# Optimization experiments

Measured on AMD Instinct MI355X. Metric: run time of the kernel, lower is better.

The kernel has to match this reference:

```python
import math
import jax, jax.numpy as jnp
import numpy as np

B, S, M, D, H, FF = 2, 2048, 64, 1024, 16, 4096
HD = D // H


def setup_inputs() -> dict:
    key = jax.random.key(0)
    ks = jax.random.split(key, 16)
    w = lambda k, shape: jax.random.normal(k, shape, dtype=jnp.float32) * 0.02
    # RoPE angles: theta_i = pos / 10000^(2i/head_dim)
    inv_freq = 1.0 / (10000.0 ** (jnp.arange(0, HD, 2, dtype=jnp.float32) / HD))
    ang = jnp.arange(S, dtype=jnp.float32)[:, None] * inv_freq[None, :]  # (S, HD//2)
    return {
        "tgt": jax.random.normal(ks[0], (B, S, D), dtype=jnp.float32),
        "memory": jax.random.normal(ks[1], (B, M, D), dtype=jnp.float32),
        "rope_cos": jnp.cos(ang),
        "rope_sin": jnp.sin(ang),
        "W_qkv": w(ks[2], (D, 3 * D)), "b_qkv": jnp.zeros((3 * D,), jnp.float32),
        "W_o": w(ks[3], (D, D)), "b_o": jnp.zeros((D,), jnp.float32),
        "Wq_c": w(ks[4], (D, D)), "bq_c": jnp.zeros((D,), jnp.float32),
        "Wk_c": w(ks[5], (D, D)), "bk_c": jnp.zeros((D,), jnp.float32),
        "Wv_c": w(ks[6], (D, D)), "bv_c": jnp.zeros((D,), jnp.float32),
        "W_co": w(ks[7], (D, D)), "b_co": jnp.zeros((D,), jnp.float32),
        "W1": w(ks[8], (D, FF)), "b1": jnp.zeros((FF,), jnp.float32),
        "W2": w(ks[9], (FF, D)), "b2": jnp.zeros((D,), jnp.float32),
        "g1": jnp.ones((D,), jnp.float32), "be1": jnp.zeros((D,), jnp.float32),
        "g2": jnp.ones((D,), jnp.float32), "be2": jnp.zeros((D,), jnp.float32),
        "g3": jnp.ones((D,), jnp.float32), "be3": jnp.zeros((D,), jnp.float32),
    }


def _layer_norm(x, g, b, eps=1e-5):
    mu = jnp.mean(x, axis=-1, keepdims=True)
    var = jnp.mean(jnp.square(x - mu), axis=-1, keepdims=True)
    return (x - mu) * jax.lax.rsqrt(var + eps) * g + b


def _apply_rope(x, cos, sin):
    # x: (B, H, S, HD); cos/sin: (S, HD//2). Pairs (even, odd) rotated as complex.
    xe, xo = x[..., 0::2], x[..., 1::2]
    c = cos[None, None]
    s = sin[None, None]
    re = xe * c - xo * s
    im = xe * s + xo * c
    return jnp.stack([re, im], axis=-1).reshape(x.shape)


def reference(tgt, memory, rope_cos, rope_sin, W_qkv, b_qkv, W_o, b_o,
              Wq_c, bq_c, Wk_c, bk_c, Wv_c, bv_c, W_co, b_co,
              W1, b1, W2, b2, g1, be1, g2, be2, g3, be3):
    b, s, d = tgt.shape
    scale = 1.0 / math.sqrt(HD)

    # --- RoPE self-attention (causal) ---
    x = _layer_norm(tgt, g1, be1)
    qkv = (x @ W_qkv + b_qkv).reshape(b, s, 3, H, HD)
    qkv = jnp.transpose(qkv, (2, 0, 3, 1, 4))  # (3, b, H, s, HD)
    q, k, v = qkv[0], qkv[1], qkv[2]
    q = _apply_rope(q, rope_cos[:s], rope_sin[:s])
    k = _apply_rope(k, rope_cos[:s], rope_sin[:s])
    attn = jnp.einsum('bhqd,bhkd->bhqk', q, k) * scale
    causal = jnp.tril(jnp.ones((s, s), dtype=bool))
    attn = jnp.where(causal[None, None], attn, -1e9)
    attn = jax.nn.softmax(attn, axis=-1)
    sa = jnp.einsum('bhqk,bhkd->bhqd', attn, v)
    sa = jnp.transpose(sa, (0, 2, 1, 3)).reshape(b, s, d)
    tgt = tgt + (sa @ W_o + b_o)

    # --- cross-attention to memory (no positional encoding) ---
    x = _layer_norm(tgt, g2, be2)
    m = memory.shape[1]
    qc = (x @ Wq_c + bq_c).reshape(b, s, H, HD).transpose(0, 2, 1, 3)
    kc = (memory @ Wk_c + bk_c).reshape(b, m, H, HD).transpose(0, 2, 1, 3)
    vc = (memory @ Wv_c + bv_c).reshape(b, m, H, HD).transpose(0, 2, 1, 3)
    ca = jax.nn.softmax(jnp.einsum('bhqd,bhkd->bhqk', qc, kc) * scale, axis=-1)
    co = jnp.einsum('bhqk,bhkd->bhqd', ca, vc)
    co = jnp.transpose(co, (0, 2, 1, 3)).reshape(b, s, d)
    tgt = tgt + (co @ W_co + b_co)

    # --- FFN (exact GELU, dropout disabled = eval) ---
    x = _layer_norm(tgt, g3, be3)
    ffn = jax.nn.gelu(x @ W1 + b1, approximate=False) @ W2 + b2
    return tgt + ffn
```

## Files before the change

kernel.cpp:

```cpp
#include <hip/hip_runtime.h>

typedef unsigned short u16;
typedef short bf16x8 __attribute__((ext_vector_type(8)));
typedef float f32x4 __attribute__((ext_vector_type(4)));

#define HN 16
#define SD 64
#define SEQ 2048
#define DM 1024
#define QSC 0.18033688f

__device__ __forceinline__ float bf2f(u16 h) {
  return __uint_as_float(((unsigned int)h) << 16);
}
__device__ __forceinline__ u16 f2bf(float f) {
  unsigned int x = __float_as_uint(f);
  x += 0x7fffu + ((x >> 16) & 1u);
  return (u16)(x >> 16);
}
__device__ __forceinline__ float geluf(float x) {
  return 0.5f * x * (1.0f + erff(x * 0.70710678118654752f));
}
__device__ __forceinline__ void load_lds16(const u16* g, u16* l) {
  __builtin_amdgcn_global_load_lds(
      (const __attribute__((address_space(1))) void*)g,
      (__attribute__((address_space(3))) void*)l, 16, 0, 0);
}
__device__ __forceinline__ unsigned ldsoff(const u16* p) {
  return (unsigned)(unsigned long long)(
      const __attribute__((address_space(3))) u16*)p;
}

__device__ __forceinline__ void trans_tile(const float* __restrict__ in,
                                           u16* __restrict__ out, int K, int N,
                                           int tx, int ty, int tid,
                                           u16 (*T)[72]) {
  const int n0 = tx * 64, k0 = ty * 64;
#pragma unroll
  for (int it = 0; it < 2; ++it) {
    const int t = it * 256 + tid, r = t >> 3, c = (t & 7) * 8;
    const float* src = &in[(size_t)(k0 + r) * N + n0 + c];
    float4 d0 = *(const float4*)src;
    float4 d1 = *(const float4*)(src + 4);
    T[r][c + 0] = f2bf(d0.x);
    T[r][c + 1] = f2bf(d0.y);
    T[r][c + 2] = f2bf(d0.z);
    T[r][c + 3] = f2bf(d0.w);
    T[r][c + 4] = f2bf(d1.x);
    T[r][c + 5] = f2bf(d1.y);
    T[r][c + 6] = f2bf(d1.z);
    T[r][c + 7] = f2bf(d1.w);
  }
  __syncthreads();
#pragma unroll
  for (int it = 0; it < 2; ++it) {
    const int t = it * 256 + tid, r = t >> 3, c = (t & 7) * 8;
    uint4 d;
    u16* p = (u16*)&d;
#pragma unroll
    for (int j = 0; j < 8; ++j) p[j] = T[c + j][r];
    *(uint4*)&out[(size_t)(n0 + r) * K + k0 + c] = d;
  }
}

__global__ __launch_bounds__(256) void prep1(
    const float* __restrict__ Wqkv, const float* __restrict__ Wo,
    const float* __restrict__ Wqc, const float* __restrict__ Wkc,
    const float* __restrict__ Wvc, const float* __restrict__ Wco,
    u16* __restrict__ Tqkv, u16* __restrict__ To, u16* __restrict__ Tqc,
    u16* __restrict__ Tkc, u16* __restrict__ Tvc, u16* __restrict__ Tco,
    const float* __restrict__ mem, u16* __restrict__ memb) {
  __shared__ u16 T[64][72];
  const int t = blockIdx.x, tid = threadIdx.x;
  if (t < 768) {
    trans_tile(Wqkv, Tqkv, 1024, 3072, t % 48, t / 48, tid, T);
    return;
  }
  if (t < 2048) {
    const int u = t - 768, m = u >> 8, sub = u & 255;
    const float* in;
    u16* out;
    if (m == 0) { in = Wo; out = To; }
    else if (m == 1) { in = Wqc; out = Tqc; }
    else if (m == 2) { in = Wkc; out = Tkc; }
    else if (m == 3) { in = Wvc; out = Tvc; }
    else { in = Wco; out = Tco; }
    trans_tile(in, out, 1024, 1024, sub & 15, sub >> 4, tid, T);
    return;
  }
  const int i = ((t - 2048) * 256 + tid) * 4;
  float4 d = *(const float4*)&mem[i];
  uint2 o;
  u16* po = (u16*)&o;
  po[0] = f2bf(d.x);
  po[1] = f2bf(d.y);
  po[2] = f2bf(d.z);
  po[3] = f2bf(d.w);
  *(uint2*)&memb[i] = o;
}

__global__ __launch_bounds__(256) void prep2(const float* __restrict__ W1,
                                             const float* __restrict__ W2,
                                             u16* __restrict__ T1,
                                             u16* __restrict__ T2) {
  __shared__ u16 T[64][72];
  const int t = blockIdx.x, tid = threadIdx.x;
  if (t < 1024) {
    trans_tile(W1, T1, 1024, 4096, t & 63, t >> 6, tid, T);
  } else {
    const int u = t - 1024;
    trans_tile(W2, T2, 4096, 1024, u & 15, u >> 4, tid, T);
  }
}

__global__ __launch_bounds__(256) void ln_kernel(
    const float* __restrict__ x, const float* __restrict__ g,
    const float* __restrict__ be, u16* __restrict__ y) {
  const int row = blockIdx.x, tid = threadIdx.x;
  const float* xr = x + (size_t)row * DM;
  float4 d = *(const float4*)&xr[tid * 4];
  float v[4] = {d.x, d.y, d.z, d.w};
  float s1 = 0.f, s2 = 0.f;
#pragma unroll
  for (int j = 0; j < 4; ++j) {
    s1 += v[j];
    s2 += v[j] * v[j];
  }
#pragma unroll
  for (int dd = 1; dd < 64; dd <<= 1) {
    s1 += __shfl_xor(s1, dd, 64);
    s2 += __shfl_xor(s2, dd, 64);
  }
  __shared__ float p1[4], p2[4];
  const int lane = tid & 63, wv = tid >> 6;
  if (lane == 0) {
    p1[wv] = s1;
    p2[wv] = s2;
  }
  __syncthreads();
  s1 = p1[0] + p1[1] + p1[2] + p1[3];
  s2 = p2[0] + p2[1] + p2[2] + p2[3];
  const float mu = s1 * (1.f / DM);
  const float rs = rsqrtf(fmaxf(s2 * (1.f / DM) - mu * mu, 0.f) + 1e-5f);
  float4 gg = *(const float4*)&g[tid * 4];
  float4 bb = *(const float4*)&be[tid * 4];
  const float gv[4] = {gg.x, gg.y, gg.z, gg.w};
  const float bv[4] = {bb.x, bb.y, bb.z, bb.w};
  uint2 o;
  u16* po = (u16*)&o;
#pragma unroll
  for (int j = 0; j < 4; ++j) po[j] = f2bf((v[j] - mu) * rs * gv[j] + bv[j]);
  *(uint2*)&y[(size_t)row * DM + tid * 4] = o;
}

template <int EPI, int TM>
__global__ __launch_bounds__(256) void gemm_bt(
    const u16* __restrict__ A, const u16* __restrict__ Bt,
    const float* __restrict__ bias, const float* __restrict__ resid,
    void* __restrict__ C0, u16* __restrict__ C1, u16* __restrict__ C2, int M,
    int N, int K, int rpbl, float sc, const float* __restrict__ rcos,
    const float* __restrict__ rsin) {
  constexpr int MI = TM / 32;
  __shared__ __align__(16) u16 As[TM][64];
  __shared__ __align__(16) u16 Bs[128][64];
  const int tid = threadIdx.x;
  const int lane = tid & 63, wv = tid >> 6;
  const int l16 = lane & 15, quad = lane >> 4;

  if (EPI == 6 && blockIdx.z) {
    Bt = (const u16*)C1;
    bias = resid;
  }

  int bx = blockIdx.x, by = blockIdx.y;
  const int gx = gridDim.x, gy = gridDim.y;
  if ((gy & 7) == 0) {
    const int f = by * gx + bx;
    const int c = f & 7, j = f >> 3;
    const int jm = j / gx;
    by = c * (gy >> 3) + jm;
    bx = j - jm * gx;
  }
  const int m0 = by * TM, n0 = bx * 128;
  const int wm = (wv >> 1) * (TM / 2), wn = (wv & 1) * 64;

  const int srow = lane >> 3;
  const int sblk = (lane & 7) ^ srow;
  const u16* ag[MI];
  const u16* bg[4];
  u16* la[MI];
  u16* lb[4];
#pragma unroll
  for (int i = 0; i < MI; ++i) {
    const int r0 = i * 32 + wv * 8;
    ag[i] = A + (size_t)(m0 + r0 + srow) * K + sblk * 8;
    la[i] = &As[r0][0] + lane * 8;
  }
#pragma unroll
  for (int i = 0; i < 4; ++i) {
    const int r0 = i * 32 + wv * 8;
    bg[i] = Bt + (size_t)(n0 + r0 + srow) * K + sblk * 8;
    lb[i] = &Bs[r0][0] + lane * 8;
  }

  f32x4 acc[MI][4] = {};

  for (int k0 = 0; k0 < K; k0 += 64) {
    __syncthreads();
#pragma unroll
    for (int i = 0; i < MI; ++i) load_lds16(ag[i] + k0, la[i]);
#pragma unroll
    for (int i = 0; i < 4; ++i) load_lds16(bg[i] + k0, lb[i]);
    __syncthreads();
#pragma unroll
    for (int kk = 0; kk < 2; ++kk) {
      bf16x8 af[MI], bfr[4];
#pragma unroll
      for (int mi = 0; mi < MI; ++mi) {
        const int row = wm + mi * 16 + l16;
        const int blk = (kk * 4 + quad) ^ (row & 7);
        af[mi] = *(const bf16x8*)&As[row][blk * 8];
      }
#pragma unroll
      for (int ni = 0; ni < 4; ++ni) {
        const int row = wn + ni * 16 + l16;
        const int blk = (kk * 4 + quad) ^ (row & 7);
        bfr[ni] = *(const bf16x8*)&Bs[row][blk * 8];
      }
#pragma unroll
      for (int mi = 0; mi < MI; ++mi)
#pragma unroll
        for (int ni = 0; ni < 4; ++ni)
          acc[mi][ni] = __builtin_amdgcn_mfma_f32_16x16x32_bf16(
              af[mi], bfr[ni], acc[mi][ni], 0, 0, 0);
    }
  }

  const int SL = 1 << rpbl;
#pragma unroll
  for (int mi = 0; mi < MI; ++mi) {
#pragma unroll
    for (int ni = 0; ni < 4; ++ni) {
#pragma unroll
      for (int r = 0; r < 4; ++r) {
        const int row = m0 + wm + mi * 16 + quad * 4 + r;
        const int col = n0 + wn + ni * 16 + l16;
        float vv = acc[mi][ni][r] + bias[col];
        if (EPI == 1) {
          vv += resid[(size_t)row * N + col];
          ((float*)C0)[(size_t)row * N + col] = vv;
        } else if (EPI == 2) {
          ((u16*)C0)[(size_t)row * N + col] = f2bf(geluf(vv));
        } else if (EPI == 3) {
          const float partner = __shfl_xor(vv, 1);
          const int which = col >> 10;
          const int nn = col & 1023;
          const int h = nn >> 6, hd = nn & 63;
          const int b = row >> rpbl;
          const int s = row & (SL - 1);
          if (which == 2) {
            C2[(((size_t)b * HN + h) * SD + hd) * SL + s] = f2bf(vv);
          } else {
            const int p = hd >> 1;
            const float cv = rcos[s * 32 + p];
            const float sv2 = rsin[s * 32 + p];
            float o = (hd & 1) ? (partner * sv2 + vv * cv)
                               : (vv * cv - partner * sv2);
            if (which == 0) o *= QSC;
            u16* dst = (which == 0) ? (u16*)C0 : C1;
            dst[(((size_t)b * HN + h) * SL + s) * SD + hd] = f2bf(o);
          }
        } else if (EPI == 4) {
          vv *= sc;
          const int h = col >> 6, hd = col & 63;
          const int b = row >> rpbl;
          const int s = row & (SL - 1);
          ((u16*)C0)[(((size_t)b * HN + h) * SL + s) * SD + hd] = f2bf(vv);
        } else if (EPI == 5) {
          const int h = col >> 6, hd = col & 63;
          const int b = row >> rpbl;
          const int s = row & (SL - 1);
          ((u16*)C0)[(((size_t)b * HN + h) * SD + hd) * SL + s] = f2bf(vv);
        } else if (EPI == 6) {
          const int h = col >> 6, hd = col & 63;
          const int b = row >> rpbl;
          const int s = row & (SL - 1);
          if (blockIdx.z == 0)
            ((u16*)C0)[(((size_t)b * HN + h) * SL + s) * SD + hd] = f2bf(vv);
          else
            C2[(((size_t)b * HN + h) * SD + hd) * SL + s] = f2bf(vv);
        } else {
          ((u16*)C0)[(size_t)row * N + col] = f2bf(vv);
        }
      }
    }
  }
}

template <int EPI>
__global__ __launch_bounds__(512, 2) void gemm8p(
    const u16* __restrict__ A, const u16* __restrict__ Bt,
    const float* __restrict__ bias, void* __restrict__ C0,
    u16* __restrict__ C1, u16* __restrict__ C2, int M, int N, int K, int rpbl,
    const float* __restrict__ rcos, const float* __restrict__ rsin) {
  __shared__ __align__(16) u16 L[4][2][8192];
  const int tid = threadIdx.x;
  const int lane = tid & 63, wv = tid >> 6;
  const int l16 = lane & 15, quad = lane >> 4;
  int bx = blockIdx.x, by = blockIdx.y;
  {
    const int gx = gridDim.x;
    const int nwg = gx * gridDim.y;
    if ((nwg & 7) == 0) {
      const int f = by * gx + bx;
      const int q = nwg >> 3;
      const int wg = (f & 7) * q + (f >> 3);
      by = wg / gx;
      bx = wg - by * gx;
    }
  }
  const int m0 = by * 256, n0 = bx * 256;
  const int wm = (wv >> 2) * 128, wn = (wv & 3) * 64;
  const int nk = K >> 6;

  const u16* Ag = A + (size_t)m0 * K;
  const u16* Bg = Bt + (size_t)n0 * K;

#define STAGE(MAT, H, ST, P)                                                  \
  {                                                                           \
    const int tt = (ST) < nk ? (ST) : nk - 1;         \
    const int k0s = tt << 6;                                                  \
    u16* dst = &L[(MAT)*2 + (H)][P][0];                                       \
    const u16* srcp = (MAT) ? Bg : Ag;                                        \
    _Pragma("unroll") for (int j = 0; j < 2; ++j) {                           \
      const int li = wv * 2 + j;                                              \
      const int pr = li * 8 + (lane >> 3);                                    \
      const int bb = lane & 7;                                                \
      const int gg2 = bb ^ (pr & 7);                                          \
      const int rw = 2 * pr + (gg2 >> 2);                                     \
      load_lds16(srcp + (size_t)rw * K + k0s + (H)*32 + (gg2 & 3) * 8,        \
                 dst + li * 512 + lane * 8);                                  \
    }                                                                         \
  }

  unsigned aaddr[2][4], baddr[4];
  {
    const unsigned Lb = ldsoff(&L[0][0][0]);
#pragma unroll
    for (int MH = 0; MH < 2; ++MH)
#pragma unroll
      for (int mi = 0; mi < 4; ++mi) {
        const int R = wm + MH * 64 + mi * 16 + l16;
        const int p = R >> 1, g = (R & 1) * 4 + quad, b = g ^ (p & 7);
        aaddr[MH][mi] = Lb + (unsigned)(p * 64 + b * 8) * 2u;
      }
#pragma unroll
    for (int ni = 0; ni < 4; ++ni) {
      const int R = wn + ni * 16 + l16;
      const int p = R >> 1, g = (R & 1) * 4 + quad, b = g ^ (p & 7);
      baddr[ni] = Lb + 65536u + (unsigned)(p * 64 + b * 8) * 2u;
    }
  }

  f32x4 acc[8][4] = {};
  bf16x8 bfr[4];

#define PHASE(CB, KK, MH, RB, SM, SH, ST, SP, VM)                             \
  {                                                                           \
    bf16x8 af[4];                                                             \
    _Pragma("unroll") for (int mi = 0; mi < 4; ++mi)                          \
        asm volatile("ds_read_b128 %0, %1 offset:%2"                          \
                     : "=v"(af[mi])                                           \
                     : "v"(aaddr[MH][mi]), "i"((KK)*32768 + (CB)*16384));     \
    if (RB) {                                                                 \
      _Pragma("unroll") for (int ni = 0; ni < 4; ++ni)                        \
          asm volatile("ds_read_b128 %0, %1 offset:%2"                        \
                       : "=v"(bfr[ni])                                        \
                       : "v"(baddr[ni]), "i"((KK)*32768 + (CB)*16384));       \
    }                                                                         \
    STAGE(SM, SH, ST, SP);                                                    \
    __builtin_amdgcn_s_barrier();                                             \
    asm volatile("s_waitcnt lgkmcnt(0)");                                     \
    __builtin_amdgcn_sched_barrier(0);                                        \
    __builtin_amdgcn_s_setprio(1);                                            \
    _Pragma("unroll") for (int mi = 0; mi < 4; ++mi)                          \
        _Pragma("unroll") for (int ni = 0; ni < 4; ++ni) acc[(MH)*4 + mi]     \
            [ni] = __builtin_amdgcn_mfma_f32_16x16x32_bf16(                   \
                af[mi], bfr[ni], acc[(MH)*4 + mi][ni], 0, 0, 0);              \
    __builtin_amdgcn_s_setprio(0);                                            \
    if (VM) asm volatile("s_waitcnt vmcnt(8)");                               \
    __builtin_amdgcn_s_barrier();                                             \
  }

  STAGE(0, 0, 0, 0);
  STAGE(1, 0, 0, 0);
  STAGE(0, 1, 0, 0);
  STAGE(1, 1, 0, 0);
  STAGE(0, 0, 1, 1);
  STAGE(1, 0, 1, 1);
  asm volatile("s_waitcnt vmcnt(8)");
  __builtin_amdgcn_s_barrier();

  for (int t = 0; t < nk; t += 2) {
    PHASE(0, 0, 0, true, 0, 1, t + 1, 1, false)
    PHASE(0, 0, 1, false, 1, 1, t + 1, 1, true)
    PHASE(0, 1, 0, true, 0, 0, t + 2, 0, false)
    PHASE(0, 1, 1, false, 1, 0, t + 2, 0, true)
    PHASE(1, 0, 0, true, 0, 1, t + 2, 0, false)
    PHASE(1, 0, 1, false, 1, 1, t + 2, 0, true)
    PHASE(1, 1, 0, true, 0, 0, t + 3, 1, false)
    PHASE(1, 1, 1, false, 1, 0, t + 3, 1, true)
  }
#undef PHASE
#undef STAGE

  const int SL = 1 << rpbl;
#pragma unroll
  for (int mi = 0; mi < 8; ++mi) {
#pragma unroll
    for (int ni = 0; ni < 4; ++ni) {
#pragma unroll
      for (int r = 0; r < 4; ++r) {
        const int row = m0 + wm + mi * 16 + quad * 4 + r;
        const int col = n0 + wn + ni * 16 + l16;
        float vv = acc[mi][ni][r] + bias[col];
        if (EPI == 2) {
          ((u16*)C0)[(size_t)row * N + col] = f2bf(geluf(vv));
        } else if (EPI == 3) {
          const float partner = __shfl_xor(vv, 1);
          const int which = col >> 10;
          const int nn = col & 1023;
          const int h = nn >> 6, hd = nn & 63;
          const int b = row >> rpbl;
          const int s = row & (SL - 1);
          if (which == 2) {
            C2[(((size_t)b * HN + h) * SD + hd) * SL + s] = f2bf(vv);
          } else {
            const int p = hd >> 1;
            const float cv = rcos[s * 32 + p];
            const float sv2 = rsin[s * 32 + p];
            float o = (hd & 1) ? (partner * sv2 + vv * cv)
                               : (vv * cv - partner * sv2);
            if (which == 0) o *= QSC;
            u16* dst = (which == 0) ? (u16*)C0 : C1;
            dst[(((size_t)b * HN + h) * SL + s) * SD + hd] = f2bf(o);
          }
        } else {
          ((u16*)C0)[(size_t)row * N + col] = f2bf(vv);
        }
      }
    }
  }
}

template <int CAUSAL>
__global__ __launch_bounds__(512, 4) void attn_kernel(
    const u16* __restrict__ q, const u16* __restrict__ k,
    const u16* __restrict__ vt, u16* __restrict__ out, int kv_len) {
  __shared__ u16 Qs[128][72], Ks[64][72], VTs[64][72];
  __shared__ u16 Ps[128][68];
  const int tid = threadIdx.x;
  const int lane = tid & 63, wv = tid >> 6;
  const int t2 = wv >> 2, w4 = wv & 3;
  const int l16 = lane & 15, quad = lane >> 4;
  const int bx = blockIdx.x, bh = blockIdx.y;
  const int qtA = bx;
  const int qtB = CAUSAL ? (31 - bx) : (bx + 16);
  const int qt = t2 ? qtB : qtA;
  const u16* qb = q + (size_t)bh * SEQ * SD;
  const u16* kb = k + (size_t)bh * kv_len * SD;
  const u16* vtb = vt + (size_t)bh * SD * kv_len;

#pragma unroll
  for (int it = 0; it < 2; ++it) {
    const int t = it * 512 + tid, r = t >> 3, c = (t & 7) * 8;
    const int qrow = (r < 64) ? (qtA * 64 + r) : (qtB * 64 + (r - 64));
    *(uint4*)&Qs[r][c] = *(const uint4*)&qb[(size_t)qrow * SD + c];
  }

  f32x4 o_acc[4] = {};
  float l_i[4] = {};

  const int ktiles = CAUSAL ? (qtB + 1) : ((kv_len + 63) >> 6);
  const int sr = tid >> 3, sc8 = (tid & 7) * 8;

  for (int kt = 0; kt < ktiles; ++kt) {
    const uint4 kd = *(const uint4*)&kb[((size_t)kt * 64 + sr) * SD + sc8];
    const uint4 vd = *(const uint4*)&vtb[(size_t)sr * kv_len + kt * 64 + sc8];
    __syncthreads();
    *(uint4*)&Ks[sr][sc8] = kd;
    *(uint4*)&VTs[sr][sc8] = vd;
    __syncthreads();

    if (kt <= qt) {
      const int roff = t2 * 64 + w4 * 16;
      f32x4 s_acc[4] = {};
#pragma unroll
      for (int kk = 0; kk < 64; kk += 32) {
        const bf16x8 aq = *(const bf16x8*)&Qs[roff + l16][kk + quad * 8];
#pragma unroll
        for (int ni = 0; ni < 4; ++ni) {
          const bf16x8 bk = *(const bf16x8*)&Ks[ni * 16 + l16][kk + quad * 8];
          s_acc[ni] = __builtin_amdgcn_mfma_f32_16x16x32_bf16(aq, bk, s_acc[ni],
                                                              0, 0, 0);
        }
      }
      float rsum[4] = {0.f, 0.f, 0.f, 0.f};
      const bool dg = CAUSAL && (kt == qt);
#pragma unroll
      for (int ni = 0; ni < 4; ++ni)
#pragma unroll
        for (int r = 0; r < 4; ++r) {
          float sv = s_acc[ni][r];
          if (dg && (ni * 16 + l16 > w4 * 16 + quad * 4 + r)) sv = -1e9f;
          const float pe = __builtin_amdgcn_exp2f(sv);
          rsum[r] += pe;
          Ps[wv * 16 + quad * 4 + r][ni * 16 + l16] =
              (u16)(__float_as_uint(pe) >> 16);
        }
#pragma unroll
      for (int r = 0; r < 4; ++r) {
#pragma unroll
        for (int dd = 1; dd < 16; dd <<= 1)
          rsum[r] += __shfl_xor(rsum[r], dd, 64);
        l_i[r] += rsum[r];
      }
#pragma unroll
      for (int kk = 0; kk < 64; kk += 32) {
        const bf16x8 ap = *(const bf16x8*)&Ps[wv * 16 + l16][kk + quad * 8];
#pragma unroll
        for (int ni = 0; ni < 4; ++ni) {
          const bf16x8 bv = *(const bf16x8*)&VTs[ni * 16 + l16][kk + quad * 8];
          o_acc[ni] = __builtin_amdgcn_mfma_f32_16x16x32_bf16(ap, bv, o_acc[ni],
                                                              0, 0, 0);
        }
      }
    }
  }

  const int b = bh >> 4, h = bh & 15;
#pragma unroll
  for (int r = 0; r < 4; ++r) {
    const float inv = 1.f / l_i[r];
    const int s = qt * 64 + w4 * 16 + quad * 4 + r;
#pragma unroll
    for (int ni = 0; ni < 4; ++ni)
      out[((size_t)b * SEQ + s) * DM + h * SD + ni * 16 + l16] =
          f2bf(o_acc[ni][r] * inv);
  }
}

extern "C" void kernel_launch(void* const* d_in, const int* in_sizes, int n_in,
                              void* d_out, int out_size, void* d_ws,
                              size_t ws_size, hipStream_t stream) {
  (void)in_sizes;
  (void)n_in;
  (void)out_size;
  (void)ws_size;
  const float* tgt = (const float*)d_in[0];
  const float* mem = (const float*)d_in[1];
  const float* rc = (const float*)d_in[2];
  const float* rsn = (const float*)d_in[3];
  const float* W_qkv = (const float*)d_in[4];
  const float* b_qkv = (const float*)d_in[5];
  const float* W_o = (const float*)d_in[6];
  const float* b_o = (const float*)d_in[7];
  const float* Wq_c = (const float*)d_in[8];
  const float* bq_c = (const float*)d_in[9];
  const float* Wk_c = (const float*)d_in[10];
  const float* bk_c = (const float*)d_in[11];
  const float* Wv_c = (const float*)d_in[12];
  const float* bv_c = (const float*)d_in[13];
  const float* W_co = (const float*)d_in[14];
  const float* b_co = (const float*)d_in[15];
  const float* W1 = (const float*)d_in[16];
  const float* b1 = (const float*)d_in[17];
  const float* W2 = (const float*)d_in[18];
  const float* b2 = (const float*)d_in[19];
  const float* g1 = (const float*)d_in[20];
  const float* be1 = (const float*)d_in[21];
  const float* g2 = (const float*)d_in[22];
  const float* be2 = (const float*)d_in[23];
  const float* g3 = (const float*)d_in[24];
  const float* be3 = (const float*)d_in[25];

  const size_t M1 = 1048576;
  u16* w = (u16*)d_ws;
  u16* WTqkv = w;
  u16* WTo = w + 3 * M1;
  u16* WTqc = w + 4 * M1;
  u16* WTkc = w + 5 * M1;
  u16* WTvc = w + 6 * M1;
  u16* WTco = w + 7 * M1;
  u16* WT1 = w;
  u16* WT2 = w + 4 * M1;
  u16* xb = w + 8 * M1;
  u16* qb = w + 12 * M1;
  u16* kb = w + 16 * M1;
  u16* vbT = w + 20 * M1;
  u16* at = w + 24 * M1;
  u16* kc = w + 28 * M1;
  u16* vcT = kc + 131072;
  u16* memb = vcT + 131072;
  u16* ffh = qb;
  float* res = (float*)d_out;

  dim3 blk(256), blk512(512);
  prep1<<<2176, blk, 0, stream>>>(W_qkv, W_o, Wq_c, Wk_c, Wv_c, W_co, WTqkv,
                                  WTo, WTqc, WTkc, WTvc, WTco, mem, memb);

  ln_kernel<<<4096, blk, 0, stream>>>(tgt, g1, be1, xb);
  gemm8p<3><<<dim3(12, 16), blk512, 0, stream>>>(xb, WTqkv, b_qkv, qb, kb, vbT,
                                                 4096, 3072, 1024, 11, rc, rsn);
  attn_kernel<1><<<dim3(16, 32), blk512, 0, stream>>>(qb, kb, vbT, at, 2048);
  gemm_bt<1, 64><<<dim3(8, 64), blk, 0, stream>>>(at, WTo, b_o, tgt, res,
                                                  nullptr, nullptr, 4096, 1024,
                                                  1024, 0, 1.f, nullptr,
                                                  nullptr);
  ln_kernel<<<4096, blk, 0, stream>>>(res, g2, be2, xb);
  gemm_bt<4, 64><<<dim3(8, 64), blk, 0, stream>>>(
      xb, WTqc, bq_c, nullptr, qb, nullptr, nullptr, 4096, 1024, 1024, 11, QSC,
      nullptr, nullptr);
  gemm_bt<6, 64><<<dim3(8, 2, 2), blk, 0, stream>>>(
      memb, WTkc, bk_c, bv_c, kc, WTvc, vcT, 128, 1024, 1024, 6, 1.f, nullptr,
      nullptr);
  attn_kernel<0><<<dim3(16, 32), blk512, 0, stream>>>(qb, kc, vcT, at, 64);
  gemm_bt<1, 64><<<dim3(8, 64), blk, 0, stream>>>(at, WTco, b_co, res, res,
                                                  nullptr, nullptr, 4096, 1024,
                                                  1024, 0, 1.f, nullptr,
                                                  nullptr);
  prep2<<<2048, blk, 0, stream>>>(W1, W2, WT1, WT2);
  ln_kernel<<<4096, blk, 0, stream>>>(res, g3, be3, xb);
  gemm8p<2><<<dim3(16, 16), blk512, 0, stream>>>(xb, WT1, b1, ffh, nullptr,
                                                 nullptr, 4096, 4096, 1024, 0,
                                                 nullptr, nullptr);
  gemm_bt<1, 64><<<dim3(8, 64), blk, 0, stream>>>(ffh, WT2, b2, res, res,
                                                  nullptr, nullptr, 4096, 1024,
                                                  4096, 0, 1.f, nullptr,
                                                  nullptr);
}
```

Before: 490.1 us.

## Template wide GEMM on N-fragments, use 192-wide tiles for QKV, merge phases

```diff
diff --git a/kernel.cpp b/kernel.cpp
--- a/kernel.cpp
+++ b/kernel.cpp
@@ -297,7 +297,7 @@
   }
 }
 
-template <int EPI>
+template <int EPI, int NI>
 __global__ __launch_bounds__(512, 2) void gemm8p(
     const u16* __restrict__ A, const u16* __restrict__ Bt,
     const float* __restrict__ bias, void* __restrict__ C0,
@@ -319,8 +319,8 @@
       bx = wg - by * gx;
     }
   }
-  const int m0 = by * 256, n0 = bx * 256;
-  const int wm = (wv >> 2) * 128, wn = (wv & 3) * 64;
+  const int m0 = by * 256, n0 = bx * (NI * 64);
+  const int wm = (wv >> 2) * 128, wn = (wv & 3) * (NI * 16);
   const int nk = K >> 6;
 
   const u16* Ag = A + (size_t)m0 * K;
@@ -343,7 +343,7 @@
     }                                                                         \
   }
 
-  unsigned aaddr[2][4], baddr[4];
+  unsigned aaddr[2][4], baddr[NI];
   {
     const unsigned Lb = ldsoff(&L[0][0][0]);
 #pragma unroll
@@ -355,40 +355,43 @@
         aaddr[MH][mi] = Lb + (unsigned)(p * 64 + b * 8) * 2u;
       }
 #pragma unroll
-    for (int ni = 0; ni < 4; ++ni) {
+    for (int ni = 0; ni < NI; ++ni) {
       const int R = wn + ni * 16 + l16;
       const int p = R >> 1, g = (R & 1) * 4 + quad, b = g ^ (p & 7);
       baddr[ni] = Lb + 65536u + (unsigned)(p * 64 + b * 8) * 2u;
     }
   }
 
-  f32x4 acc[8][4] = {};
-  bf16x8 bfr[4];
-
-#define PHASE(CB, KK, MH, RB, SM, SH, ST, SP, VM)                             \
+  f32x4 acc[8][NI] = {};
+
+#define PHASE(CB, KK, S1M, S1H, S2M, S2H, ST, SP)                             \
   {                                                                           \
-    bf16x8 af[4];                                                             \
-    _Pragma("unroll") for (int mi = 0; mi < 4; ++mi)                          \
+    bf16x8 af[2][4];                                                          \
+    bf16x8 bfr[NI];                                                           \
+    _Pragma("unroll") for (int mh = 0; mh < 2; ++mh)                          \
+        _Pragma("unroll") for (int mi = 0; mi < 4; ++mi)                      \
+            asm volatile("ds_read_b128 %0, %1 offset:%2"                      \
+                         : "=v"(af[mh][mi])                                   \
+                         : "v"(aaddr[mh][mi]),                                \
+                           "i"((KK)*32768 + (CB)*16384));                     \
+    _Pragma("unroll") for (int ni = 0; ni < NI; ++ni)                         \
         asm volatile("ds_read_b128 %0, %1 offset:%2"                          \
-                     : "=v"(af[mi])                                           \
-                     : "v"(aaddr[MH][mi]), "i"((KK)*32768 + (CB)*16384));     \
-    if (RB) {                                                                 \
-      _Pragma("unroll") for (int ni = 0; ni < 4; ++ni)                        \
-          asm volatile("ds_read_b128 %0, %1 offset:%2"                        \
-                       : "=v"(bfr[ni])                                        \
-                       : "v"(baddr[ni]), "i"((KK)*32768 + (CB)*16384));       \
-    }                                                                         \
-    STAGE(SM, SH, ST, SP);                                                    \
+                     : "=v"(bfr[ni])                                          \
+                     : "v"(baddr[ni]), "i"((KK)*32768 + (CB)*16384));         \
+    STAGE(S1M, S1H, ST, SP);                                                  \
+    STAGE(S2M, S2H, ST, SP);                                                  \
     __builtin_amdgcn_s_barrier();                                             \
     asm volatile("s_waitcnt lgkmcnt(0)");                                     \
     __builtin_amdgcn_sched_barrier(0);                                        \
     __builtin_amdgcn_s_setprio(1);                                            \
-    _Pragma("unroll") for (int mi = 0; mi < 4; ++mi)                          \
-        _Pragma("unroll") for (int ni = 0; ni < 4; ++ni) acc[(MH)*4 + mi]     \
-            [ni] = __builtin_amdgcn_mfma_f32_16x16x32_bf16(                   \
-                af[mi], bfr[ni], acc[(MH)*4 + mi][ni], 0, 0, 0);              \
+    _Pragma("unroll") for (int mh = 0; mh < 2; ++mh)                          \
+        _Pragma("unroll") for (int mi = 0; mi < 4; ++mi)                      \
+            _Pragma("unroll") for (int ni = 0; ni < NI; ++ni)                 \
+                acc[mh * 4 + mi][ni] =                                        \
+                    __builtin_amdgcn_mfma_f32_16x16x32_bf16(                  \
+                        af[mh][mi], bfr[ni], acc[mh * 4 + mi][ni], 0, 0, 0);  \
     __builtin_amdgcn_s_setprio(0);                                            \
-    if (VM) asm volatile("s_waitcnt vmcnt(8)");                               \
+    asm volatile("s_waitcnt vmcnt(8)");                                       \
     __builtin_amdgcn_s_barrier();                                             \
   }
 
@@ -402,14 +405,10 @@
   __builtin_amdgcn_s_barrier();
 
   for (int t = 0; t < nk; t += 2) {
-    PHASE(0, 0, 0, true, 0, 1, t + 1, 1, false)
-    PHASE(0, 0, 1, false, 1, 1, t + 1, 1, true)
-    PHASE(0, 1, 0, true, 0, 0, t + 2, 0, false)
-    PHASE(0, 1, 1, false, 1, 0, t + 2, 0, true)
-    PHASE(1, 0, 0, true, 0, 1, t + 2, 0, false)
-    PHASE(1, 0, 1, false, 1, 1, t + 2, 0, true)
-    PHASE(1, 1, 0, true, 0, 0, t + 3, 1, false)
-    PHASE(1, 1, 1, false, 1, 0, t + 3, 1, true)
+    PHASE(0, 0, 0, 1, 1, 1, t + 1, 1)
+    PHASE(0, 1, 0, 0, 1, 0, t + 2, 0)
+    PHASE(1, 0, 0, 1, 1, 1, t + 2, 0)
+    PHASE(1, 1, 0, 0, 1, 0, t + 3, 1)
   }
 #undef PHASE
 #undef STAGE
@@ -418,7 +417,7 @@
 #pragma unroll
   for (int mi = 0; mi < 8; ++mi) {
 #pragma unroll
-    for (int ni = 0; ni < 4; ++ni) {
+    for (int ni = 0; ni < NI; ++ni) {
 #pragma unroll
       for (int r = 0; r < 4; ++r) {
         const int row = m0 + wm + mi * 16 + quad * 4 + r;
@@ -610,8 +609,8 @@
                                   WTo, WTqc, WTkc, WTvc, WTco, mem, memb);
 
   ln_kernel<<<4096, blk, 0, stream>>>(tgt, g1, be1, xb);
-  gemm8p<3><<<dim3(12, 16), blk512, 0, stream>>>(xb, WTqkv, b_qkv, qb, kb, vbT,
-                                                 4096, 3072, 1024, 11, rc, rsn);
+  gemm8p<3, 3><<<dim3(16, 16), blk512, 0, stream>>>(
+      xb, WTqkv, b_qkv, qb, kb, vbT, 4096, 3072, 1024, 11, rc, rsn);
   attn_kernel<1><<<dim3(16, 32), blk512, 0, stream>>>(qb, kb, vbT, at, 2048);
   gemm_bt<1, 64><<<dim3(8, 64), blk, 0, stream>>>(at, WTo, b_o, tgt, res,
                                                   nullptr, nullptr, 4096, 1024,
@@ -631,9 +630,9 @@
                                                   nullptr);
   prep2<<<2048, blk, 0, stream>>>(W1, W2, WT1, WT2);
   ln_kernel<<<4096, blk, 0, stream>>>(res, g3, be3, xb);
-  gemm8p<2><<<dim3(16, 16), blk512, 0, stream>>>(xb, WT1, b1, ffh, nullptr,
-                                                 nullptr, 4096, 4096, 1024, 0,
-                                                 nullptr, nullptr);
+  gemm8p<2, 4><<<dim3(16, 16), blk512, 0, stream>>>(xb, WT1, b1, ffh, nullptr,
+                                                    nullptr, 4096, 4096, 1024,
+                                                    0, nullptr, nullptr);
   gemm_bt<1, 64><<<dim3(8, 64), blk, 0, stream>>>(ffh, WT2, b2, res, res,
                                                   nullptr, nullptr, 4096, 1024,
                                                   4096, 0, 1.f, nullptr,
```

Measured after the change: 493.3 us. No clear change (+0.6%).
